# Kernel tuning notes

Hardware: AMD Instinct MI355X
Metric: run time of the kernel (lower is better)

The kernel has to match this reference:

```python
import jax, jax.numpy as jnp
import numpy as np

P = 15          # processor layers
D = 128         # node/edge feature dim (== hidden dim)
N_NODES = 10000
N_EDGES = 160000


def _mlp(x, w0, b0, w1, b1, w2, b2):
    h = jax.nn.relu(x @ w0 + b0)
    h = jax.nn.relu(h @ w1 + b1)
    return h @ w2 + b2


def setup_inputs() -> dict:
    key = jax.random.key(0)
    ks = jax.random.split(key, 20)
    inp = {
        "node_features": jax.random.normal(ks[0], (N_NODES, D), jnp.float32),
        "edge_features": jax.random.normal(ks[1], (N_EDGES, D), jnp.float32),
        "src": jax.random.randint(ks[2], (N_EDGES,), 0, N_NODES, jnp.int32),
        "dst": jax.random.randint(ks[3], (N_EDGES,), 0, N_NODES, jnp.int32),
    }
    s = 0.05
    # edge MLP: input 2*D + D = 384 -> 128 -> 128 -> 128, stacked over P layers
    inp["ew0"] = jax.random.normal(ks[4], (P, 3 * D, D), jnp.float32) * s
    inp["eb0"] = jnp.zeros((P, D), jnp.float32)
    inp["ew1"] = jax.random.normal(ks[5], (P, D, D), jnp.float32) * s
    inp["eb1"] = jnp.zeros((P, D), jnp.float32)
    inp["ew2"] = jax.random.normal(ks[6], (P, D, D), jnp.float32) * s
    inp["eb2"] = jnp.zeros((P, D), jnp.float32)
    # node MLP: input D + D = 256 -> 128 -> 128 -> 128
    inp["nw0"] = jax.random.normal(ks[7], (P, 2 * D, D), jnp.float32) * s
    inp["nb0"] = jnp.zeros((P, D), jnp.float32)
    inp["nw1"] = jax.random.normal(ks[8], (P, D, D), jnp.float32) * s
    inp["nb1"] = jnp.zeros((P, D), jnp.float32)
    inp["nw2"] = jax.random.normal(ks[9], (P, D, D), jnp.float32) * s
    inp["nb2"] = jnp.zeros((P, D), jnp.float32)
    return inp


def reference(node_features, edge_features, src, dst,
              ew0, eb0, ew1, eb1, ew2, eb2,
              nw0, nb0, nw1, nb1, nw2, nb2):
    n, e = node_features, edge_features
    for i in range(P):
        # --- edge block: gather src/dst node feats, edge MLP, residual ---
        cat_e = jnp.concatenate([n[src], n[dst], e], axis=-1)  # [E, 3D]
        e = _mlp(cat_e, ew0[i], eb0[i], ew1[i], eb1[i], ew2[i], eb2[i]) + e
        # --- node block: scatter-sum edges to dst nodes, node MLP, residual ---
        agg = jax.ops.segment_sum(e, dst, num_segments=N_NODES)  # [N, D]
        cat_n = jnp.concatenate([n, agg], axis=-1)               # [N, 2D]
        n = _mlp(cat_n, nw0[i], nb0[i], nw1[i], nb1[i], nw2[i], nb2[i]) + n
    return n
```

## Files before the change

kernel.cpp:

```cpp
#include <hip/hip_runtime.h>

#define DD 128
#define PP 15
#define NNODES 10000
#define NEDGES 160000

typedef __attribute__((ext_vector_type(8))) short bf16x8;
typedef __attribute__((ext_vector_type(4))) float f32x4;

__device__ inline ushort f2bf(float f) {
  unsigned u = __builtin_bit_cast(unsigned, f);
  u += 0x7FFFu + ((u >> 16) & 1u);
  return (ushort)(u >> 16);
}

__device__ inline float bf2f(ushort h) {
  unsigned u = ((unsigned)h) << 16;
  return __builtin_bit_cast(float, u);
}

__device__ inline uint cvt_pk(float lo, float hi) {
  uint r;
  asm("v_cvt_pk_bf16_f32 %0, %1, %2" : "=v"(r) : "v"(lo), "v"(hi));
  return r;
}

__device__ inline f32x4 mfma16(bf16x8 a, bf16x8 b, f32x4 c) {
  return __builtin_amdgcn_mfma_f32_16x16x32_bf16(a, b, c, 0, 0, 0);
}

__global__ __launch_bounds__(256) void pack_all(
    const float* __restrict__ ew0, const float* __restrict__ ew1,
    const float* __restrict__ ew2, const float* __restrict__ nw0,
    const float* __restrict__ nw1, const float* __restrict__ nw2,
    ushort* __restrict__ out) {
  int i = blockIdx.x * 256 + threadIdx.x;
  if (i >= 2211840) return;
  const float* w; int K; int j = i;
  if (i < 737280)       { w = ew0; K = 384; }
  else if (i < 983040)  { w = ew1; K = 128; j = i - 737280; }
  else if (i < 1228800) { w = ew2; K = 128; j = i - 983040; }
  else if (i < 1720320) { w = nw0; K = 256; j = i - 1228800; }
  else if (i < 1966080) { w = nw1; K = 128; j = i - 1720320; }
  else                  { w = nw2; K = 128; j = i - 1966080; }
  int per = K * 128;
  int p = j / per, q = j % per;
  int e = q & 7;
  int lane = (q >> 3) & 63;
  int t = q >> 9;
  int nkt = K >> 5;
  int kt = t % nkt, cb = t / nkt;
  int k = kt * 32 + ((lane >> 4) << 3) + e;
  int n = (cb << 4) + (lane & 15);
  out[i] = f2bf(w[(size_t)p * per + (size_t)k * 128 + n]);
}

__global__ __launch_bounds__(256) void cvt_all(const float* __restrict__ ef,
                                               const float* __restrict__ nf,
                                               ushort* __restrict__ ebf,
                                               float* __restrict__ nbuf,
                                               ushort* __restrict__ nbf) {
  const int en4 = NEDGES * DD / 4;
  const int nn4 = NNODES * DD / 4;
  int i = blockIdx.x * 256 + threadIdx.x;
  if (i < en4) {
    float4 v = ((const float4*)ef)[i];
    ushort4 h;
    h.x = f2bf(v.x); h.y = f2bf(v.y); h.z = f2bf(v.z); h.w = f2bf(v.w);
    ((ushort4*)ebf)[i] = h;
  } else if (i < en4 + nn4) {
    int k = i - en4;
    float4 v = ((const float4*)nf)[k];
    ((float4*)nbuf)[k] = v;
    ushort4 h;
    h.x = f2bf(v.x); h.y = f2bf(v.y); h.z = f2bf(v.z); h.w = f2bf(v.w);
    ((ushort4*)nbf)[k] = h;
  }
}

__global__ __launch_bounds__(256) void hist_kernel(const int* __restrict__ dst,
                                                   int* __restrict__ cnt) {
  int i = blockIdx.x * 256 + threadIdx.x;
  if (i < NEDGES) atomicAdd(&cnt[dst[i]], 1);
}

__global__ __launch_bounds__(256) void scan_kernel(const int* __restrict__ cnt,
                                                   int* __restrict__ row_start,
                                                   int* __restrict__ cursor) {
  __shared__ int part[256];
  const int CH = (NNODES + 255) / 256;
  int t = threadIdx.x;
  int beg = t * CH, end = min(beg + CH, NNODES);
  int s = 0;
  for (int i = beg; i < end; ++i) s += cnt[i];
  part[t] = s;
  __syncthreads();
  for (int off = 1; off < 256; off <<= 1) {
    int v = (t >= off) ? part[t - off] : 0;
    __syncthreads();
    part[t] += v;
    __syncthreads();
  }
  int run = part[t] - s;
  for (int i = beg; i < end; ++i) {
    row_start[i] = run;
    cursor[i] = run;
    run += cnt[i];
  }
  if (t == 255) row_start[NNODES] = NEDGES;
}

__global__ __launch_bounds__(256) void scatter_kernel(const int* __restrict__ dst,
                                                      int* __restrict__ cursor,
                                                      int* __restrict__ eidx) {
  int i = blockIdx.x * 256 + threadIdx.x;
  if (i < NEDGES) {
    int pos = atomicAdd(&cursor[dst[i]], 1);
    eidx[pos] = i;
  }
}

__global__ __launch_bounds__(256) void agg_kernel(const ushort* __restrict__ ebf,
                                                  ushort* __restrict__ abf,
                                                  const int* __restrict__ row_start,
                                                  const int* __restrict__ eidx) {
  int wv = threadIdx.x >> 6, lane = threadIdx.x & 63;
  int node = blockIdx.x * 4 + wv;
  if (node >= NNODES) return;
  int jb = row_start[node], je = row_start[node + 1];
  float ax = 0.f, ay = 0.f, bx = 0.f, by = 0.f;
  float cx = 0.f, cy = 0.f, dx = 0.f, dy = 0.f;
  int j = jb;
  for (; j + 3 < je; j += 4) {
    int e0 = eidx[j], e1 = eidx[j + 1], e2 = eidx[j + 2], e3 = eidx[j + 3];
    uint u0 = *(const uint*)(ebf + (size_t)e0 * DD + lane * 2);
    uint u1 = *(const uint*)(ebf + (size_t)e1 * DD + lane * 2);
    uint u2 = *(const uint*)(ebf + (size_t)e2 * DD + lane * 2);
    uint u3 = *(const uint*)(ebf + (size_t)e3 * DD + lane * 2);
    ax += bf2f((ushort)u0); ay += __builtin_bit_cast(float, u0 & 0xFFFF0000u);
    bx += bf2f((ushort)u1); by += __builtin_bit_cast(float, u1 & 0xFFFF0000u);
    cx += bf2f((ushort)u2); cy += __builtin_bit_cast(float, u2 & 0xFFFF0000u);
    dx += bf2f((ushort)u3); dy += __builtin_bit_cast(float, u3 & 0xFFFF0000u);
  }
  for (; j < je; ++j) {
    int e0 = eidx[j];
    uint u0 = *(const uint*)(ebf + (size_t)e0 * DD + lane * 2);
    ax += bf2f((ushort)u0); ay += __builtin_bit_cast(float, u0 & 0xFFFF0000u);
  }
  float sx = (ax + bx) + (cx + dx);
  float sy = (ay + by) + (cy + dy);
  *(uint*)&abf[(size_t)node * DD + lane * 2] = cvt_pk(sx, sy);
}

__global__ __launch_bounds__(256) void edge_kernel(
    const ushort* __restrict__ nbf, ushort* __restrict__ ebf,
    const int* __restrict__ srcI, const int* __restrict__ dstI,
    const ushort* __restrict__ w0, const float* __restrict__ b0,
    const ushort* __restrict__ w1, const float* __restrict__ b1,
    const ushort* __restrict__ w2, const float* __restrict__ b2) {
  __shared__ ushort Elds[32 * 128];
  __shared__ ushort Hlds[32 * 128];
  const int tid = threadIdx.x;
  const int e0 = blockIdx.x * 32;
  const int lane = tid & 63, wv = tid >> 6;
  const int l15 = lane & 15, l4 = lane >> 4;

#pragma unroll
  for (int i = 0; i < 2; ++i) {
    int c = i * 256 + tid;
    int row = c >> 4, f8 = c & 15;
    bf16x8 v = *(const bf16x8*)(ebf + (size_t)(e0 + row) * DD + f8 * 8);
    *(bf16x8*)&Elds[row * 128 + ((f8 ^ (row & 15)) * 8)] = v;
  }

  const ushort* sp0 = nbf + (size_t)srcI[e0 + l15] * DD + l4 * 8;
  const ushort* sp1 = nbf + (size_t)srcI[e0 + 16 + l15] * DD + l4 * 8;
  const ushort* dp0 = nbf + (size_t)dstI[e0 + l15] * DD + l4 * 8;
  const ushort* dp1 = nbf + (size_t)dstI[e0 + 16 + l15] * DD + l4 * 8;
  __syncthreads();

  const f32x4 z = {0.f, 0.f, 0.f, 0.f};
  const int cbA = wv * 2, cbB = wv * 2 + 1;
  f32x4 acc[2][2];
  acc[0][0] = z; acc[0][1] = z; acc[1][0] = z; acc[1][1] = z;

#pragma unroll
  for (int kt = 0; kt < 4; ++kt) {
    bf16x8 bA = *(const bf16x8*)(w0 + (size_t)((cbA * 12 + kt) * 64 + lane) * 8);
    bf16x8 bB = *(const bf16x8*)(w0 + (size_t)((cbB * 12 + kt) * 64 + lane) * 8);
    bf16x8 a0 = *(const bf16x8*)(sp0 + kt * 32);
    bf16x8 a1 = *(const bf16x8*)(sp1 + kt * 32);
    acc[0][0] = mfma16(a0, bA, acc[0][0]); acc[0][1] = mfma16(a0, bB, acc[0][1]);
    acc[1][0] = mfma16(a1, bA, acc[1][0]); acc[1][1] = mfma16(a1, bB, acc[1][1]);
  }
#pragma unroll
  for (int kt = 0; kt < 4; ++kt) {
    bf16x8 bA = *(const bf16x8*)(w0 + (size_t)((cbA * 12 + 4 + kt) * 64 + lane) * 8);
    bf16x8 bB = *(const bf16x8*)(w0 + (size_t)((cbB * 12 + 4 + kt) * 64 + lane) * 8);
    bf16x8 a0 = *(const bf16x8*)(dp0 + kt * 32);
    bf16x8 a1 = *(const bf16x8*)(dp1 + kt * 32);
    acc[0][0] = mfma16(a0, bA, acc[0][0]); acc[0][1] = mfma16(a0, bB, acc[0][1]);
    acc[1][0] = mfma16(a1, bA, acc[1][0]); acc[1][1] = mfma16(a1, bB, acc[1][1]);
  }
#pragma unroll
  for (int kt = 0; kt < 4; ++kt) {
    bf16x8 bA = *(const bf16x8*)(w0 + (size_t)((cbA * 12 + 8 + kt) * 64 + lane) * 8);
    bf16x8 bB = *(const bf16x8*)(w0 + (size_t)((cbB * 12 + 8 + kt) * 64 + lane) * 8);
    int sl = ((kt * 4 + l4) ^ l15) * 8;
    bf16x8 a0 = *(const bf16x8*)&Elds[l15 * 128 + sl];
    bf16x8 a1 = *(const bf16x8*)&Elds[(16 + l15) * 128 + sl];
    acc[0][0] = mfma16(a0, bA, acc[0][0]); acc[0][1] = mfma16(a0, bB, acc[0][1]);
    acc[1][0] = mfma16(a1, bA, acc[1][0]); acc[1][1] = mfma16(a1, bB, acc[1][1]);
  }

  {
    float biasA = b0[cbA * 16 + l15], biasB = b0[cbB * 16 + l15];
#pragma unroll
    for (int cbi = 0; cbi < 2; ++cbi) {
      int col = (wv * 2 + cbi) * 16 + l15;
      float bias = cbi ? biasB : biasA;
      int cs = col >> 3, c7 = col & 7;
#pragma unroll
      for (int rb = 0; rb < 2; ++rb) {
        float v0 = fmaxf(acc[rb][cbi][0] + bias, 0.f);
        float v1 = fmaxf(acc[rb][cbi][1] + bias, 0.f);
        float v2 = fmaxf(acc[rb][cbi][2] + bias, 0.f);
        float v3 = fmaxf(acc[rb][cbi][3] + bias, 0.f);
        uint p01 = cvt_pk(v0, v1), p23 = cvt_pk(v2, v3);
        int r0 = rb * 16 + l4 * 4;
        Hlds[(r0 + 0) * 128 + ((cs ^ ((r0 + 0) & 15)) * 8) + c7] = (ushort)p01;
        Hlds[(r0 + 1) * 128 + ((cs ^ ((r0 + 1) & 15)) * 8) + c7] = (ushort)(p01 >> 16);
        Hlds[(r0 + 2) * 128 + ((cs ^ ((r0 + 2) & 15)) * 8) + c7] = (ushort)p23;
        Hlds[(r0 + 3) * 128 + ((cs ^ ((r0 + 3) & 15)) * 8) + c7] = (ushort)(p23 >> 16);
      }
    }
  }
  __syncthreads();

  acc[0][0] = z; acc[0][1] = z; acc[1][0] = z; acc[1][1] = z;
#pragma unroll
  for (int kt = 0; kt < 4; ++kt) {
    bf16x8 bA = *(const bf16x8*)(w1 + (size_t)((cbA * 4 + kt) * 64 + lane) * 8);
    bf16x8 bB = *(const bf16x8*)(w1 + (size_t)((cbB * 4 + kt) * 64 + lane) * 8);
    int sl = ((kt * 4 + l4) ^ l15) * 8;
    bf16x8 a0 = *(const bf16x8*)&Hlds[l15 * 128 + sl];
    bf16x8 a1 = *(const bf16x8*)&Hlds[(16 + l15) * 128 + sl];
    acc[0][0] = mfma16(a0, bA, acc[0][0]); acc[0][1] = mfma16(a0, bB, acc[0][1]);
    acc[1][0] = mfma16(a1, bA, acc[1][0]); acc[1][1] = mfma16(a1, bB, acc[1][1]);
  }
  uint h2p[2][2][2];
  {
    float biasA = b1[cbA * 16 + l15], biasB = b1[cbB * 16 + l15];
#pragma unroll
    for (int cbi = 0; cbi < 2; ++cbi) {
      float bias = cbi ? biasB : biasA;
#pragma unroll
      for (int rb = 0; rb < 2; ++rb) {
        float v0 = fmaxf(acc[rb][cbi][0] + bias, 0.f);
        float v1 = fmaxf(acc[rb][cbi][1] + bias, 0.f);
        float v2 = fmaxf(acc[rb][cbi][2] + bias, 0.f);
        float v3 = fmaxf(acc[rb][cbi][3] + bias, 0.f);
        h2p[rb][cbi][0] = cvt_pk(v0, v1);
        h2p[rb][cbi][1] = cvt_pk(v2, v3);
      }
    }
  }
  __syncthreads();
  {
#pragma unroll
    for (int cbi = 0; cbi < 2; ++cbi) {
      int col = (wv * 2 + cbi) * 16 + l15;
      int cs = col >> 3, c7 = col & 7;
#pragma unroll
      for (int rb = 0; rb < 2; ++rb) {
        uint p01 = h2p[rb][cbi][0], p23 = h2p[rb][cbi][1];
        int r0 = rb * 16 + l4 * 4;
        Hlds[(r0 + 0) * 128 + ((cs ^ ((r0 + 0) & 15)) * 8) + c7] = (ushort)p01;
        Hlds[(r0 + 1) * 128 + ((cs ^ ((r0 + 1) & 15)) * 8) + c7] = (ushort)(p01 >> 16);
        Hlds[(r0 + 2) * 128 + ((cs ^ ((r0 + 2) & 15)) * 8) + c7] = (ushort)p23;
        Hlds[(r0 + 3) * 128 + ((cs ^ ((r0 + 3) & 15)) * 8) + c7] = (ushort)(p23 >> 16);
      }
    }
  }
  __syncthreads();

  acc[0][0] = z; acc[0][1] = z; acc[1][0] = z; acc[1][1] = z;
#pragma unroll
  for (int kt = 0; kt < 4; ++kt) {
    bf16x8 bA = *(const bf16x8*)(w2 + (size_t)((cbA * 4 + kt) * 64 + lane) * 8);
    bf16x8 bB = *(const bf16x8*)(w2 + (size_t)((cbB * 4 + kt) * 64 + lane) * 8);
    int sl = ((kt * 4 + l4) ^ l15) * 8;
    bf16x8 a0 = *(const bf16x8*)&Hlds[l15 * 128 + sl];
    bf16x8 a1 = *(const bf16x8*)&Hlds[(16 + l15) * 128 + sl];
    acc[0][0] = mfma16(a0, bA, acc[0][0]); acc[0][1] = mfma16(a0, bB, acc[0][1]);
    acc[1][0] = mfma16(a1, bA, acc[1][0]); acc[1][1] = mfma16(a1, bB, acc[1][1]);
  }
  {
#pragma unroll
    for (int cbi = 0; cbi < 2; ++cbi) {
      int col = (wv * 2 + cbi) * 16 + l15;
      float bias = b2[col];
      int cs = col >> 3, c7 = col & 7;
#pragma unroll
      for (int rb = 0; rb < 2; ++rb) {
        int r0 = rb * 16 + l4 * 4;
        int i0 = (r0 + 0) * 128 + ((cs ^ ((r0 + 0) & 15)) * 8) + c7;
        int i1 = (r0 + 1) * 128 + ((cs ^ ((r0 + 1) & 15)) * 8) + c7;
        int i2 = (r0 + 2) * 128 + ((cs ^ ((r0 + 2) & 15)) * 8) + c7;
        int i3 = (r0 + 3) * 128 + ((cs ^ ((r0 + 3) & 15)) * 8) + c7;
        float v0 = bf2f(Elds[i0]) + acc[rb][cbi][0] + bias;
        float v1 = bf2f(Elds[i1]) + acc[rb][cbi][1] + bias;
        float v2 = bf2f(Elds[i2]) + acc[rb][cbi][2] + bias;
        float v3 = bf2f(Elds[i3]) + acc[rb][cbi][3] + bias;
        uint p01 = cvt_pk(v0, v1), p23 = cvt_pk(v2, v3);
        Elds[i0] = (ushort)p01;
        Elds[i1] = (ushort)(p01 >> 16);
        Elds[i2] = (ushort)p23;
        Elds[i3] = (ushort)(p23 >> 16);
      }
    }
  }
  __syncthreads();
#pragma unroll
  for (int i = 0; i < 2; ++i) {
    int c = i * 256 + tid;
    int row = c >> 4, f8 = c & 15;
    bf16x8 v = *(const bf16x8*)&Elds[row * 128 + ((f8 ^ (row & 15)) * 8)];
    *(bf16x8*)&ebf[(size_t)(e0 + row) * DD + f8 * 8] = v;
  }
}

__global__ __launch_bounds__(256) void node_kernel(
    float* __restrict__ nbuf, ushort* __restrict__ nbf,
    const ushort* __restrict__ abf,
    const ushort* __restrict__ w0, const float* __restrict__ b0,
    const ushort* __restrict__ w1, const float* __restrict__ b1,
    const ushort* __restrict__ w2, const float* __restrict__ b2) {
  __shared__ ushort Alds[32 * 256];
  __shared__ ushort Hlds[32 * 128];
  const int tid = threadIdx.x;
  const int n0 = blockIdx.x * 32;
  const int lane = tid & 63, wv = tid >> 6;
  const int l15 = lane & 15, l4 = lane >> 4;

#pragma unroll
  for (int i = 0; i < 4; ++i) {
    int c = i * 256 + tid;
    int row = c >> 5, f8 = c & 31;
    int node = n0 + row;
    bf16x8 v = {0, 0, 0, 0, 0, 0, 0, 0};
    if (node < NNODES) {
      const ushort* sp = (f8 < 16) ? nbf + (size_t)node * DD + f8 * 8
                                   : abf + (size_t)node * DD + (f8 - 16) * 8;
      v = *(const bf16x8*)sp;
    }
    *(bf16x8*)&Alds[row * 256 + ((f8 ^ (row & 15)) * 8)] = v;
  }
  __syncthreads();

  const f32x4 z = {0.f, 0.f, 0.f, 0.f};
  const int cbA = wv * 2, cbB = wv * 2 + 1;
  f32x4 acc[2][2];

  acc[0][0] = z; acc[0][1] = z; acc[1][0] = z; acc[1][1] = z;
#pragma unroll
  for (int kt = 0; kt < 8; ++kt) {
    bf16x8 bA = *(const bf16x8*)(w0 + (size_t)((cbA * 8 + kt) * 64 + lane) * 8);
    bf16x8 bB = *(const bf16x8*)(w0 + (size_t)((cbB * 8 + kt) * 64 + lane) * 8);
    int sl = ((kt * 4 + l4) ^ l15) * 8;
    bf16x8 a0 = *(const bf16x8*)&Alds[l15 * 256 + sl];
    bf16x8 a1 = *(const bf16x8*)&Alds[(16 + l15) * 256 + sl];
    acc[0][0] = mfma16(a0, bA, acc[0][0]); acc[0][1] = mfma16(a0, bB, acc[0][1]);
    acc[1][0] = mfma16(a1, bA, acc[1][0]); acc[1][1] = mfma16(a1, bB, acc[1][1]);
  }
  {
    float biasA = b0[cbA * 16 + l15], biasB = b0[cbB * 16 + l15];
#pragma unroll
    for (int cbi = 0; cbi < 2; ++cbi) {
      int col = (wv * 2 + cbi) * 16 + l15;
      float bias = cbi ? biasB : biasA;
      int cs = col >> 3, c7 = col & 7;
#pragma unroll
      for (int rb = 0; rb < 2; ++rb) {
        float v0 = fmaxf(acc[rb][cbi][0] + bias, 0.f);
        float v1 = fmaxf(acc[rb][cbi][1] + bias, 0.f);
        float v2 = fmaxf(acc[rb][cbi][2] + bias, 0.f);
        float v3 = fmaxf(acc[rb][cbi][3] + bias, 0.f);
        uint p01 = cvt_pk(v0, v1), p23 = cvt_pk(v2, v3);
        int r0 = rb * 16 + l4 * 4;
        Hlds[(r0 + 0) * 128 + ((cs ^ ((r0 + 0) & 15)) * 8) + c7] = (ushort)p01;
        Hlds[(r0 + 1) * 128 + ((cs ^ ((r0 + 1) & 15)) * 8) + c7] = (ushort)(p01 >> 16);
        Hlds[(r0 + 2) * 128 + ((cs ^ ((r0 + 2) & 15)) * 8) + c7] = (ushort)p23;
        Hlds[(r0 + 3) * 128 + ((cs ^ ((r0 + 3) & 15)) * 8) + c7] = (ushort)(p23 >> 16);
      }
    }
  }
  __syncthreads();

  acc[0][0] = z; acc[0][1] = z; acc[1][0] = z; acc[1][1] = z;
#pragma unroll
  for (int kt = 0; kt < 4; ++kt) {
    bf16x8 bA = *(const bf16x8*)(w1 + (size_t)((cbA * 4 + kt) * 64 + lane) * 8);
    bf16x8 bB = *(const bf16x8*)(w1 + (size_t)((cbB * 4 + kt) * 64 + lane) * 8);
    int sl = ((kt * 4 + l4) ^ l15) * 8;
    bf16x8 a0 = *(const bf16x8*)&Hlds[l15 * 128 + sl];
    bf16x8 a1 = *(const bf16x8*)&Hlds[(16 + l15) * 128 + sl];
    acc[0][0] = mfma16(a0, bA, acc[0][0]); acc[0][1] = mfma16(a0, bB, acc[0][1]);
    acc[1][0] = mfma16(a1, bA, acc[1][0]); acc[1][1] = mfma16(a1, bB, acc[1][1]);
  }
  {
    float biasA = b1[cbA * 16 + l15], biasB = b1[cbB * 16 + l15];
#pragma unroll
    for (int cbi = 0; cbi < 2; ++cbi) {
      int col = (wv * 2 + cbi) * 16 + l15;
      float bias = cbi ? biasB : biasA;
      int cs = col >> 3, c7 = col & 7;
#pragma unroll
      for (int rb = 0; rb < 2; ++rb) {
        float v0 = fmaxf(acc[rb][cbi][0] + bias, 0.f);
        float v1 = fmaxf(acc[rb][cbi][1] + bias, 0.f);
        float v2 = fmaxf(acc[rb][cbi][2] + bias, 0.f);
        float v3 = fmaxf(acc[rb][cbi][3] + bias, 0.f);
        uint p01 = cvt_pk(v0, v1), p23 = cvt_pk(v2, v3);
        int r0 = rb * 16 + l4 * 4;
        Alds[(r0 + 0) * 256 + ((16 + (cs ^ ((r0 + 0) & 15))) * 8) + c7] = (ushort)p01;
        Alds[(r0 + 1) * 256 + ((16 + (cs ^ ((r0 + 1) & 15))) * 8) + c7] = (ushort)(p01 >> 16);
        Alds[(r0 + 2) * 256 + ((16 + (cs ^ ((r0 + 2) & 15))) * 8) + c7] = (ushort)p23;
        Alds[(r0 + 3) * 256 + ((16 + (cs ^ ((r0 + 3) & 15))) * 8) + c7] = (ushort)(p23 >> 16);
      }
    }
  }
  __syncthreads();

  acc[0][0] = z; acc[0][1] = z; acc[1][0] = z; acc[1][1] = z;
#pragma unroll
  for (int kt = 0; kt < 4; ++kt) {
    bf16x8 bA = *(const bf16x8*)(w2 + (size_t)((cbA * 4 + kt) * 64 + lane) * 8);
    bf16x8 bB = *(const bf16x8*)(w2 + (size_t)((cbB * 4 + kt) * 64 + lane) * 8);
    int sl = (16 + ((kt * 4 + l4) ^ l15)) * 8;
    bf16x8 a0 = *(const bf16x8*)&Alds[l15 * 256 + sl];
    bf16x8 a1 = *(const bf16x8*)&Alds[(16 + l15) * 256 + sl];
    acc[0][0] = mfma16(a0, bA, acc[0][0]); acc[0][1] = mfma16(a0, bB, acc[0][1]);
    acc[1][0] = mfma16(a1, bA, acc[1][0]); acc[1][1] = mfma16(a1, bB, acc[1][1]);
  }
  {
#pragma unroll
    for (int cbi = 0; cbi < 2; ++cbi) {
      int col = (wv * 2 + cbi) * 16 + l15;
      float bias = b2[col];
#pragma unroll
      for (int rb = 0; rb < 2; ++rb) {
        int r0 = rb * 16 + l4 * 4;
        float res[4];
#pragma unroll
        for (int r = 0; r < 4; ++r) {
          int node = n0 + r0 + r;
          if (node < NNODES) {
            size_t off = (size_t)node * DD + col;
            res[r] = nbuf[off] + acc[rb][cbi][r] + bias;
            nbuf[off] = res[r];
          } else res[r] = 0.f;
        }
        uint p01 = cvt_pk(res[0], res[1]), p23 = cvt_pk(res[2], res[3]);
#pragma unroll
        for (int r = 0; r < 4; ++r) {
          int node = n0 + r0 + r;
          if (node < NNODES) {
            ushort h = (r == 0) ? (ushort)p01 : (r == 1) ? (ushort)(p01 >> 16)
                     : (r == 2) ? (ushort)p23 : (ushort)(p23 >> 16);
            nbf[(size_t)node * DD + col] = h;
          }
        }
      }
    }
  }
}

extern "C" void kernel_launch(void* const* d_in, const int* in_sizes, int n_in,
                              void* d_out, int out_size, void* d_ws, size_t ws_size,
                              hipStream_t stream) {
  const float* node_f = (const float*)d_in[0];
  const float* edge_f = (const float*)d_in[1];
  const int* srcI = (const int*)d_in[2];
  const int* dstI = (const int*)d_in[3];
  const float* ew0 = (const float*)d_in[4];
  const float* eb0 = (const float*)d_in[5];
  const float* ew1 = (const float*)d_in[6];
  const float* eb1 = (const float*)d_in[7];
  const float* ew2 = (const float*)d_in[8];
  const float* eb2 = (const float*)d_in[9];
  const float* nw0 = (const float*)d_in[10];
  const float* nb0 = (const float*)d_in[11];
  const float* nw1 = (const float*)d_in[12];
  const float* nb1 = (const float*)d_in[13];
  const float* nw2 = (const float*)d_in[14];
  const float* nb2 = (const float*)d_in[15];

  char* ws = (char*)d_ws;
  const size_t NB  = (size_t)NNODES * DD * 4;
  const size_t EBH = (size_t)NEDGES * DD * 2;
  const size_t NBH = (size_t)NNODES * DD * 2;
  ushort* ebf  = (ushort*)ws;
  float*  nbuf = (float*)(ws + EBH);
  ushort* nbf  = (ushort*)(ws + EBH + NB);
  ushort* abf  = (ushort*)(ws + EBH + NB + NBH);
  ushort* pw   = (ushort*)(ws + EBH + NB + 2 * NBH);
  ushort* pew0 = pw;
  ushort* pew1 = pew0 + 737280;
  ushort* pew2 = pew1 + 245760;
  ushort* pnw0 = pew2 + 245760;
  ushort* pnw1 = pnw0 + 491520;
  ushort* pnw2 = pnw1 + 245760;
  const size_t WBYTES = 2211840ull * 2;
  int* eidx      = (int*)(ws + EBH + NB + 2 * NBH + WBYTES);
  int* cnt       = eidx + NEDGES;
  int* row_start = cnt + NNODES;
  int* cursor    = row_start + NNODES + 1;

  pack_all<<<(2211840 + 255) / 256, 256, 0, stream>>>(ew0, ew1, ew2, nw0, nw1,
                                                      nw2, pw);

  hipMemsetAsync(cnt, 0, NNODES * sizeof(int), stream);
  hist_kernel<<<(NEDGES + 255) / 256, 256, 0, stream>>>(dstI, cnt);
  scan_kernel<<<1, 256, 0, stream>>>(cnt, row_start, cursor);
  scatter_kernel<<<(NEDGES + 255) / 256, 256, 0, stream>>>(dstI, cursor, eidx);

  {
    int tot = NEDGES * DD / 4 + NNODES * DD / 4;
    cvt_all<<<(tot + 255) / 256, 256, 0, stream>>>(edge_f, node_f, ebf, nbuf, nbf);
  }

  const int eblocks = NEDGES / 32;
  const int nblocks = (NNODES + 31) / 32;
  const int ablocks = (NNODES + 3) / 4;

  for (int p = 0; p < PP; ++p) {
    edge_kernel<<<eblocks, 256, 0, stream>>>(
        nbf, ebf, srcI, dstI,
        pew0 + (size_t)p * 49152, eb0 + (size_t)p * DD,
        pew1 + (size_t)p * 16384, eb1 + (size_t)p * DD,
        pew2 + (size_t)p * 16384, eb2 + (size_t)p * DD);
    agg_kernel<<<ablocks, 256, 0, stream>>>(ebf, abf, row_start, eidx);
    node_kernel<<<nblocks, 256, 0, stream>>>(
        nbuf, nbf, abf,
        pnw0 + (size_t)p * 32768, nb0 + (size_t)p * DD,
        pnw1 + (size_t)p * 16384, nb1 + (size_t)p * DD,
        pnw2 + (size_t)p * 16384, nb2 + (size_t)p * DD);
  }

  hipMemcpyAsync(d_out, nbuf, NB, hipMemcpyDeviceToDevice, stream);
}
```

Measured before the change: 1.590 ms.

## Stage gathered edge inputs in LDS and process 64 edges per block

The edge kernel now handles 64 edges per block instead of 32. It cooperatively loads the src node, dst node and edge feature rows into one swizzled 64x384 LDS tile, and runs all three MLP layers from that shared buffer. The old path read gathered node rows straight from global memory inside the MFMA loop. Each weight fragment loaded from global now feeds four row blocks instead of two, halving weight traffic per edge. The gathers become coalesced 16-byte loads, and the H2 staging reuses a separate LDS region, which removes one barrier. In exchange, each block uses 48KB of LDS and more accumulator registers, which lowers occupancy.

```diff
diff --git a/kernel.cpp b/kernel.cpp
--- a/kernel.cpp
+++ b/kernel.cpp
@@ -158,60 +158,44 @@
     const ushort* __restrict__ w0, const float* __restrict__ b0,
     const ushort* __restrict__ w1, const float* __restrict__ b1,
     const ushort* __restrict__ w2, const float* __restrict__ b2) {
-  __shared__ ushort Elds[32 * 128];
-  __shared__ ushort Hlds[32 * 128];
+  __shared__ ushort S[64 * 384];
   const int tid = threadIdx.x;
-  const int e0 = blockIdx.x * 32;
+  const int e0 = blockIdx.x * 64;
   const int lane = tid & 63, wv = tid >> 6;
   const int l15 = lane & 15, l4 = lane >> 4;
 
 #pragma unroll
-  for (int i = 0; i < 2; ++i) {
+  for (int i = 0; i < 12; ++i) {
     int c = i * 256 + tid;
-    int row = c >> 4, f8 = c & 15;
-    bf16x8 v = *(const bf16x8*)(ebf + (size_t)(e0 + row) * DD + f8 * 8);
-    *(bf16x8*)&Elds[row * 128 + ((f8 ^ (row & 15)) * 8)] = v;
-  }
-
-  const ushort* sp0 = nbf + (size_t)srcI[e0 + l15] * DD + l4 * 8;
-  const ushort* sp1 = nbf + (size_t)srcI[e0 + 16 + l15] * DD + l4 * 8;
-  const ushort* dp0 = nbf + (size_t)dstI[e0 + l15] * DD + l4 * 8;
-  const ushort* dp1 = nbf + (size_t)dstI[e0 + 16 + l15] * DD + l4 * 8;
+    int row = c / 48, f8 = c % 48;
+    const ushort* sp;
+    if (f8 < 16)       sp = nbf + (size_t)srcI[e0 + row] * DD + f8 * 8;
+    else if (f8 < 32)  sp = nbf + (size_t)dstI[e0 + row] * DD + (f8 - 16) * 8;
+    else               sp = ebf + (size_t)(e0 + row) * DD + (f8 - 32) * 8;
+    bf16x8 v = *(const bf16x8*)sp;
+    *(bf16x8*)&S[row * 384 + ((f8 ^ (row & 15)) * 8)] = v;
+  }
   __syncthreads();
 
   const f32x4 z = {0.f, 0.f, 0.f, 0.f};
   const int cbA = wv * 2, cbB = wv * 2 + 1;
-  f32x4 acc[2][2];
-  acc[0][0] = z; acc[0][1] = z; acc[1][0] = z; acc[1][1] = z;
-
-#pragma unroll
-  for (int kt = 0; kt < 4; ++kt) {
+  f32x4 acc[4][2];
+
+#pragma unroll
+  for (int rb = 0; rb < 4; ++rb) { acc[rb][0] = z; acc[rb][1] = z; }
+#pragma unroll
+  for (int kt = 0; kt < 12; ++kt) {
     bf16x8 bA = *(const bf16x8*)(w0 + (size_t)((cbA * 12 + kt) * 64 + lane) * 8);
     bf16x8 bB = *(const bf16x8*)(w0 + (size_t)((cbB * 12 + kt) * 64 + lane) * 8);
-    bf16x8 a0 = *(const bf16x8*)(sp0 + kt * 32);
-    bf16x8 a1 = *(const bf16x8*)(sp1 + kt * 32);
-    acc[0][0] = mfma16(a0, bA, acc[0][0]); acc[0][1] = mfma16(a0, bB, acc[0][1]);
-    acc[1][0] = mfma16(a1, bA, acc[1][0]); acc[1][1] = mfma16(a1, bB, acc[1][1]);
-  }
-#pragma unroll
-  for (int kt = 0; kt < 4; ++kt) {
-    bf16x8 bA = *(const bf16x8*)(w0 + (size_t)((cbA * 12 + 4 + kt) * 64 + lane) * 8);
-    bf16x8 bB = *(const bf16x8*)(w0 + (size_t)((cbB * 12 + 4 + kt) * 64 + lane) * 8);
-    bf16x8 a0 = *(const bf16x8*)(dp0 + kt * 32);
-    bf16x8 a1 = *(const bf16x8*)(dp1 + kt * 32);
-    acc[0][0] = mfma16(a0, bA, acc[0][0]); acc[0][1] = mfma16(a0, bB, acc[0][1]);
-    acc[1][0] = mfma16(a1, bA, acc[1][0]); acc[1][1] = mfma16(a1, bB, acc[1][1]);
-  }
-#pragma unroll
-  for (int kt = 0; kt < 4; ++kt) {
-    bf16x8 bA = *(const bf16x8*)(w0 + (size_t)((cbA * 12 + 8 + kt) * 64 + lane) * 8);
-    bf16x8 bB = *(const bf16x8*)(w0 + (size_t)((cbB * 12 + 8 + kt) * 64 + lane) * 8);
-    int sl = ((kt * 4 + l4) ^ l15) * 8;
-    bf16x8 a0 = *(const bf16x8*)&Elds[l15 * 128 + sl];
-    bf16x8 a1 = *(const bf16x8*)&Elds[(16 + l15) * 128 + sl];
-    acc[0][0] = mfma16(a0, bA, acc[0][0]); acc[0][1] = mfma16(a0, bB, acc[0][1]);
-    acc[1][0] = mfma16(a1, bA, acc[1][0]); acc[1][1] = mfma16(a1, bB, acc[1][1]);
-  }
+#pragma unroll
+    for (int rb = 0; rb < 4; ++rb) {
+      int row = rb * 16 + l15;
+      bf16x8 a = *(const bf16x8*)&S[row * 384 + (((kt * 4 + l4) ^ (row & 15)) * 8)];
+      acc[rb][0] = mfma16(a, bA, acc[rb][0]);
+      acc[rb][1] = mfma16(a, bB, acc[rb][1]);
+    }
+  }
+  __syncthreads();
 
   {
     float biasA = b0[cbA * 16 + l15], biasB = b0[cbB * 16 + l15];
@@ -221,79 +205,73 @@
       float bias = cbi ? biasB : biasA;
       int cs = col >> 3, c7 = col & 7;
 #pragma unroll
-      for (int rb = 0; rb < 2; ++rb) {
+      for (int rb = 0; rb < 4; ++rb) {
         float v0 = fmaxf(acc[rb][cbi][0] + bias, 0.f);
         float v1 = fmaxf(acc[rb][cbi][1] + bias, 0.f);
         float v2 = fmaxf(acc[rb][cbi][2] + bias, 0.f);
         float v3 = fmaxf(acc[rb][cbi][3] + bias, 0.f);
         uint p01 = cvt_pk(v0, v1), p23 = cvt_pk(v2, v3);
         int r0 = rb * 16 + l4 * 4;
-        Hlds[(r0 + 0) * 128 + ((cs ^ ((r0 + 0) & 15)) * 8) + c7] = (ushort)p01;
-        Hlds[(r0 + 1) * 128 + ((cs ^ ((r0 + 1) & 15)) * 8) + c7] = (ushort)(p01 >> 16);
-        Hlds[(r0 + 2) * 128 + ((cs ^ ((r0 + 2) & 15)) * 8) + c7] = (ushort)p23;
-        Hlds[(r0 + 3) * 128 + ((cs ^ ((r0 + 3) & 15)) * 8) + c7] = (ushort)(p23 >> 16);
+        S[(r0 + 0) * 384 + ((cs ^ ((r0 + 0) & 15)) * 8) + c7] = (ushort)p01;
+        S[(r0 + 1) * 384 + ((cs ^ ((r0 + 1) & 15)) * 8) + c7] = (ushort)(p01 >> 16);
+        S[(r0 + 2) * 384 + ((cs ^ ((r0 + 2) & 15)) * 8) + c7] = (ushort)p23;
+        S[(r0 + 3) * 384 + ((cs ^ ((r0 + 3) & 15)) * 8) + c7] = (ushort)(p23 >> 16);
       }
     }
   }
   __syncthreads();
 
-  acc[0][0] = z; acc[0][1] = z; acc[1][0] = z; acc[1][1] = z;
+#pragma unroll
+  for (int rb = 0; rb < 4; ++rb) { acc[rb][0] = z; acc[rb][1] = z; }
 #pragma unroll
   for (int kt = 0; kt < 4; ++kt) {
     bf16x8 bA = *(const bf16x8*)(w1 + (size_t)((cbA * 4 + kt) * 64 + lane) * 8);
     bf16x8 bB = *(const bf16x8*)(w1 + (size_t)((cbB * 4 + kt) * 64 + lane) * 8);
-    int sl = ((kt * 4 + l4) ^ l15) * 8;
-    bf16x8 a0 = *(const bf16x8*)&Hlds[l15 * 128 + sl];
-    bf16x8 a1 = *(const bf16x8*)&Hlds[(16 + l15) * 128 + sl];
-    acc[0][0] = mfma16(a0, bA, acc[0][0]); acc[0][1] = mfma16(a0, bB, acc[0][1]);
-    acc[1][0] = mfma16(a1, bA, acc[1][0]); acc[1][1] = mfma16(a1, bB, acc[1][1]);
-  }
-  uint h2p[2][2][2];
+#pragma unroll
+    for (int rb = 0; rb < 4; ++rb) {
+      int row = rb * 16 + l15;
+      bf16x8 a = *(const bf16x8*)&S[row * 384 + (((kt * 4 + l4) ^ (row & 15)) * 8)];
+      acc[rb][0] = mfma16(a, bA, acc[rb][0]);
+      acc[rb][1] = mfma16(a, bB, acc[rb][1]);
+    }
+  }
   {
     float biasA = b1[cbA * 16 + l15], biasB = b1[cbB * 16 + l15];
 #pragma unroll
     for (int cbi = 0; cbi < 2; ++cbi) {
+      int col = (wv * 2 + cbi) * 16 + l15;
       float bias = cbi ? biasB : biasA;
-#pragma unroll
-      for (int rb = 0; rb < 2; ++rb) {
+      int cs = col >> 3, c7 = col & 7;
+#pragma unroll
+      for (int rb = 0; rb < 4; ++rb) {
         float v0 = fmaxf(acc[rb][cbi][0] + bias, 0.f);
         float v1 = fmaxf(acc[rb][cbi][1] + bias, 0.f);
         float v2 = fmaxf(acc[rb][cbi][2] + bias, 0.f);
         float v3 = fmaxf(acc[rb][cbi][3] + bias, 0.f);
-        h2p[rb][cbi][0] = cvt_pk(v0, v1);
-        h2p[rb][cbi][1] = cvt_pk(v2, v3);
+        uint p01 = cvt_pk(v0, v1), p23 = cvt_pk(v2, v3);
+        int r0 = rb * 16 + l4 * 4;
+        S[(r0 + 0) * 384 + ((16 + (cs ^ ((r0 + 0) & 15))) * 8) + c7] = (ushort)p01;
+        S[(r0 + 1) * 384 + ((16 + (cs ^ ((r0 + 1) & 15))) * 8) + c7] = (ushort)(p01 >> 16);
+        S[(r0 + 2) * 384 + ((16 + (cs ^ ((r0 + 2) & 15))) * 8) + c7] = (ushort)p23;
+        S[(r0 + 3) * 384 + ((16 + (cs ^ ((r0 + 3) & 15))) * 8) + c7] = (ushort)(p23 >> 16);
       }
     }
   }
   __syncthreads();
-  {
-#pragma unroll
-    for (int cbi = 0; cbi < 2; ++cbi) {
-      int col = (wv * 2 + cbi) * 16 + l15;
-      int cs = col >> 3, c7 = col & 7;
-#pragma unroll
-      for (int rb = 0; rb < 2; ++rb) {
-        uint p01 = h2p[rb][cbi][0], p23 = h2p[rb][cbi][1];
-        int r0 = rb * 16 + l4 * 4;
-        Hlds[(r0 + 0) * 128 + ((cs ^ ((r0 + 0) & 15)) * 8) + c7] = (ushort)p01;
-        Hlds[(r0 + 1) * 128 + ((cs ^ ((r0 + 1) & 15)) * 8) + c7] = (ushort)(p01 >> 16);
-        Hlds[(r0 + 2) * 128 + ((cs ^ ((r0 + 2) & 15)) * 8) + c7] = (ushort)p23;
-        Hlds[(r0 + 3) * 128 + ((cs ^ ((r0 + 3) & 15)) * 8) + c7] = (ushort)(p23 >> 16);
-      }
-    }
-  }
-  __syncthreads();
-
-  acc[0][0] = z; acc[0][1] = z; acc[1][0] = z; acc[1][1] = z;
+
+#pragma unroll
+  for (int rb = 0; rb < 4; ++rb) { acc[rb][0] = z; acc[rb][1] = z; }
 #pragma unroll
   for (int kt = 0; kt < 4; ++kt) {
     bf16x8 bA = *(const bf16x8*)(w2 + (size_t)((cbA * 4 + kt) * 64 + lane) * 8);
     bf16x8 bB = *(const bf16x8*)(w2 + (size_t)((cbB * 4 + kt) * 64 + lane) * 8);
-    int sl = ((kt * 4 + l4) ^ l15) * 8;
-    bf16x8 a0 = *(const bf16x8*)&Hlds[l15 * 128 + sl];
-    bf16x8 a1 = *(const bf16x8*)&Hlds[(16 + l15) * 128 + sl];
-    acc[0][0] = mfma16(a0, bA, acc[0][0]); acc[0][1] = mfma16(a0, bB, acc[0][1]);
-    acc[1][0] = mfma16(a1, bA, acc[1][0]); acc[1][1] = mfma16(a1, bB, acc[1][1]);
+#pragma unroll
+    for (int rb = 0; rb < 4; ++rb) {
+      int row = rb * 16 + l15;
+      bf16x8 a = *(const bf16x8*)&S[row * 384 + ((16 + ((kt * 4 + l4) ^ (row & 15))) * 8)];
+      acc[rb][0] = mfma16(a, bA, acc[rb][0]);
+      acc[rb][1] = mfma16(a, bB, acc[rb][1]);
+    }
   }
   {
 #pragma unroll
@@ -302,30 +280,30 @@
       float bias = b2[col];
       int cs = col >> 3, c7 = col & 7;
 #pragma unroll
-      for (int rb = 0; rb < 2; ++rb) {
+      for (int rb = 0; rb < 4; ++rb) {
         int r0 = rb * 16 + l4 * 4;
-        int i0 = (r0 + 0) * 128 + ((cs ^ ((r0 + 0) & 15)) * 8) + c7;
-        int i1 = (r0 + 1) * 128 + ((cs ^ ((r0 + 1) & 15)) * 8) + c7;
-        int i2 = (r0 + 2) * 128 + ((cs ^ ((r0 + 2) & 15)) * 8) + c7;
-        int i3 = (r0 + 3) * 128 + ((cs ^ ((r0 + 3) & 15)) * 8) + c7;
-        float v0 = bf2f(Elds[i0]) + acc[rb][cbi][0] + bias;
-        float v1 = bf2f(Elds[i1]) + acc[rb][cbi][1] + bias;
-        float v2 = bf2f(Elds[i2]) + acc[rb][cbi][2] + bias;
-        float v3 = bf2f(Elds[i3]) + acc[rb][cbi][3] + bias;
+        int i0 = (r0 + 0) * 384 + ((32 + (cs ^ ((r0 + 0) & 15))) * 8) + c7;
+        int i1 = (r0 + 1) * 384 + ((32 + (cs ^ ((r0 + 1) & 15))) * 8) + c7;
+        int i2 = (r0 + 2) * 384 + ((32 + (cs ^ ((r0 + 2) & 15))) * 8) + c7;
+        int i3 = (r0 + 3) * 384 + ((32 + (cs ^ ((r0 + 3) & 15))) * 8) + c7;
+        float v0 = bf2f(S[i0]) + acc[rb][cbi][0] + bias;
+        float v1 = bf2f(S[i1]) + acc[rb][cbi][1] + bias;
+        float v2 = bf2f(S[i2]) + acc[rb][cbi][2] + bias;
+        float v3 = bf2f(S[i3]) + acc[rb][cbi][3] + bias;
         uint p01 = cvt_pk(v0, v1), p23 = cvt_pk(v2, v3);
-        Elds[i0] = (ushort)p01;
-        Elds[i1] = (ushort)(p01 >> 16);
-        Elds[i2] = (ushort)p23;
-        Elds[i3] = (ushort)(p23 >> 16);
+        S[i0] = (ushort)p01;
+        S[i1] = (ushort)(p01 >> 16);
+        S[i2] = (ushort)p23;
+        S[i3] = (ushort)(p23 >> 16);
       }
     }
   }
   __syncthreads();
 #pragma unroll
-  for (int i = 0; i < 2; ++i) {
+  for (int i = 0; i < 4; ++i) {
     int c = i * 256 + tid;
     int row = c >> 4, f8 = c & 15;
-    bf16x8 v = *(const bf16x8*)&Elds[row * 128 + ((f8 ^ (row & 15)) * 8)];
+    bf16x8 v = *(const bf16x8*)&S[row * 384 + ((32 + (f8 ^ (row & 15))) * 8)];
     *(bf16x8*)&ebf[(size_t)(e0 + row) * DD + f8 * 8] = v;
   }
 }
@@ -530,7 +508,7 @@
     cvt_all<<<(tot + 255) / 256, 256, 0, stream>>>(edge_f, node_f, ebf, nbuf, nbf);
   }
 
-  const int eblocks = NEDGES / 32;
+  const int eblocks = NEDGES / 64;
   const int nblocks = (NNODES + 31) / 32;
   const int ablocks = (NNODES + 3) / 4;
 
```

After: 1.807 ms. 1.14x slower.
